# Performance work log

Measured on AMD Instinct MI355X. Metric: run time of the kernel, lower is better.

Reference implementation:

```python
import jax, jax.numpy as jnp
import numpy as np

N_PTS = 1048576
N_FEATS = 32
GRID = (96, 96, 96)
L = 6                      # num_positional_encoding_terms
D_IN = N_FEATS + 2 * L * 3  # 68
H_DIM = 128
VMIN, VMAX = -1.0, 1.0


def setup_inputs() -> dict:
    key = jax.random.key(0)
    ks = jax.random.split(key, 5)
    def lin(k, shp, fan):
        return jax.random.normal(k, shp, jnp.float32) * (1.0 / np.sqrt(fan).astype(np.float32))
    return {
        "x": jax.random.uniform(ks[0], (N_PTS, 3), jnp.float32),          # coords in [0,1) subset of [-1,1]
        "feature_grid": jax.random.uniform(ks[1], (1, N_FEATS) + GRID, jnp.float32),
        "W0": lin(ks[2], (H_DIM, D_IN), D_IN), "b0": jnp.zeros((H_DIM,), jnp.float32),
        "W1": lin(ks[3], (H_DIM, H_DIM), H_DIM), "b1": jnp.zeros((H_DIM,), jnp.float32),
        "W2": lin(ks[4], (1, H_DIM), H_DIM), "b2": jnp.zeros((1,), jnp.float32),
    }


def positional_encoding(x):
    # x: [N, d] -> [N, 2*L*d], NeRF-style: per frequency 2^i * pi, [sin | cos]
    freqs = jnp.pi * (2.0 ** jnp.arange(L, dtype=jnp.float32))   # [L]
    xf = x[:, None, :] * freqs[None, :, None]                    # [N, L, d]
    return jnp.concatenate([jnp.sin(xf), jnp.cos(xf)], axis=-1).reshape(x.shape[0], -1)


def grid_sample_3d(grid, coords):
    # Trilinear F.grid_sample, align_corners=True.
    # grid: [C, D, H, W]; coords: [N, 3] in [-1,1], ordered (x, y, z) -> (W, H, D)
    C, D, H, W = grid.shape
    def unnorm(c, size):
        return (c + 1.0) * 0.5 * (size - 1)
    fx, fy, fz = unnorm(coords[:, 0], W), unnorm(coords[:, 1], H), unnorm(coords[:, 2], D)
    x0, y0, z0 = jnp.floor(fx), jnp.floor(fy), jnp.floor(fz)
    wx, wy, wz = fx - x0, fy - y0, fz - z0
    def ci(i, size):
        return jnp.clip(i.astype(jnp.int32), 0, size - 1)
    x0i, x1i = ci(x0, W), ci(x0 + 1, W)
    y0i, y1i = ci(y0, H), ci(y0 + 1, H)
    z0i, z1i = ci(z0, D), ci(z0 + 1, D)
    def g(zi, yi, xi):
        return grid[:, zi, yi, xi]   # irregular gather -> [C, N]
    return (g(z0i, y0i, x0i) * ((1 - wz) * (1 - wy) * (1 - wx))
          + g(z0i, y0i, x1i) * ((1 - wz) * (1 - wy) * wx)
          + g(z0i, y1i, x0i) * ((1 - wz) * wy * (1 - wx))
          + g(z0i, y1i, x1i) * ((1 - wz) * wy * wx)
          + g(z1i, y0i, x0i) * (wz * (1 - wy) * (1 - wx))
          + g(z1i, y0i, x1i) * (wz * (1 - wy) * wx)
          + g(z1i, y1i, x0i) * (wz * wy * (1 - wx))
          + g(z1i, y1i, x1i) * (wz * wy * wx))   # [C, N]


def reference(x, feature_grid, W0, b0, W1, b1, W2, b2):
    feats = grid_sample_3d(feature_grid[0], x).T                       # [N, C]
    h = jnp.concatenate([positional_encoding(x), feats], axis=1)       # [N, 68]
    h = jax.nn.relu(h @ W0.T + b0)                                     # [N, 128]
    h = jax.nn.relu(h @ W1.T + b1)                                     # [N, 128]
    y = h @ W2.T + b2                                                  # [N, 1]
    return y * (VMAX - VMIN) + VMIN
```

## Files before the change

### kernel.cpp

```cpp
#include <hip/hip_runtime.h>

#define NPTS 1048576
#define NCH 32
#define GS 96
#define GV (GS * GS * GS)
#define DIN 68
#define HD 128
#define TILE_PTS 32
#define NTILES (NPTS / TILE_PTS)
#define NBLK 256
#define NTHR 768
#define WAVES_TOT (NBLK * 12)

typedef __bf16 bf16x8 __attribute__((ext_vector_type(8)));
typedef float f32x4 __attribute__((ext_vector_type(4)));
typedef float f32x2 __attribute__((ext_vector_type(2)));

__device__ __forceinline__ unsigned int f2bf(float f) {
  unsigned int u = __float_as_uint(f);
  return (u + 0x7fffu + ((u >> 16) & 1u)) >> 16;
}
__device__ __forceinline__ unsigned int pkbf(float a, float b) {
  return f2bf(a) | (f2bf(b) << 16);
}

__global__ __launch_bounds__(256) void k_prep_grid(const float* __restrict__ src,
                                                   unsigned int* __restrict__ dst) {
  __shared__ unsigned int tile[256 * 17];
  const int tid = threadIdx.x;
  const long vb = (long)blockIdx.x * 256;
  const int c2 = tid >> 4;
  const int vgb = tid & 15;
#pragma unroll
  for (int p = 0; p < 4; ++p) {
    int vox = (vgb + p * 16) * 4;
    const float4 a = *(const float4*)(src + (long)(2 * c2) * GV + vb + vox);
    const float4 b = *(const float4*)(src + (long)(2 * c2 + 1) * GV + vb + vox);
    tile[(vox + 0) * 17 + c2] = pkbf(a.x, b.x);
    tile[(vox + 1) * 17 + c2] = pkbf(a.y, b.y);
    tile[(vox + 2) * 17 + c2] = pkbf(a.z, b.z);
    tile[(vox + 3) * 17 + c2] = pkbf(a.w, b.w);
  }
  __syncthreads();
  const int vox2 = tid >> 2;
  const int c4 = (tid & 3) * 4;
#pragma unroll
  for (int j = 0; j < 4; ++j) {
    int vx = vox2 + j * 64;
    uint4 w;
    w.x = tile[vx * 17 + c4 + 0];
    w.y = tile[vx * 17 + c4 + 1];
    w.z = tile[vx * 17 + c4 + 2];
    w.w = tile[vx * 17 + c4 + 3];
    *(uint4*)(dst + (vb + vx) * 16 + c4) = w;
  }
}

template <bool TA>
__global__ __launch_bounds__(NTHR, 3) void k_fvsrn(
    const float* __restrict__ X, const float* __restrict__ gridF,
    const unsigned short* __restrict__ gridT,
    const float* __restrict__ W0, const float* __restrict__ B0,
    const float* __restrict__ W1, const float* __restrict__ B1,
    const float* __restrict__ W2, const float* __restrict__ B2,
    float* __restrict__ out) {
  extern __shared__ char smem[];
  float* lb0 = (float*)(smem + 57344);
  float* lb1 = (float*)(smem + 57856);
  float* lw2 = (float*)(smem + 58368);
  const int tid = threadIdx.x;

  for (int idx = tid; idx < 56 * 64; idx += NTHR) {
    int f = idx >> 6;
    int L = idx & 63;
    int qq = L >> 4, lnn = L & 15;
    float vals[8];
    if (f < 24) {
      int kt = f >> 3, nt = f & 7;
      int n = nt * 16 + lnn;
      int kb = kt * 32 + qq * 8;
#pragma unroll
      for (int j = 0; j < 8; ++j) {
        int k = kb + j;
        float w = 0.f;
        if (k < 32) w = W0[n * DIN + 36 + k];
        else if (k < DIN) w = W0[n * DIN + (k - 32)];
        vals[j] = w;
      }
    } else {
      int g = f - 24;
      int kt = g >> 3, nt = g & 7;
      int n = nt * 16 + lnn;
      int kb = kt * 32 + qq * 8;
#pragma unroll
      for (int j = 0; j < 8; ++j) vals[j] = W1[n * HD + kb + j];
    }
    uint4 pk;
    pk.x = pkbf(vals[0], vals[1]);
    pk.y = pkbf(vals[2], vals[3]);
    pk.z = pkbf(vals[4], vals[5]);
    pk.w = pkbf(vals[6], vals[7]);
    *(uint4*)(smem + f * 1024 + L * 16) = pk;
  }
  if (tid < 128) lb0[tid] = B0[tid];
  else if (tid < 256) lb1[tid - 128] = B1[tid - 128];
  else if (tid < 384) lw2[tid - 256] = W2[tid - 256];
  __syncthreads();

  const int wave = tid >> 6, lane = tid & 63;
  char* scr = smem + 58880 + wave * 8192;
  const int q = lane >> 4, ln = lane & 15;
  const int half = lane >> 5, pt = lane & 31;
  const int mtg = pt >> 4, pmg = pt & 15;
  const float b2s = B2[0];

  int t = blockIdx.x * 12 + wave;
  float px = 0.f, py = 0.f, pz = 0.f;
  if (t < NTILES) {
    long p = (long)t * TILE_PTS + pt;
    px = X[p * 3 + 0]; py = X[p * 3 + 1]; pz = X[p * 3 + 2];
  }

  for (; t < NTILES;) {
    const int tn = t + WAVES_TOT;
    const long p0 = (long)t * TILE_PTS;

    float v36[36];
    {
      const float PIf = 3.14159265358979f;
      float cc[3] = {px, py, pz};
#pragma unroll
      for (int ax = 0; ax < 3; ++ax) {
        float s, co;
        __sincosf(PIf * cc[ax], &s, &co);
#pragma unroll
        for (int i = 0; i < 6; ++i) {
          v36[i * 6 + ax] = s;
          v36[i * 6 + 3 + ax] = co;
          float s2 = 2.f * s * co;
          co = 1.f - 2.f * s * s;
          s = s2;
        }
      }
    }
    unsigned int pd[8], e0, e1;
    if (half == 0) {
#pragma unroll
      for (int d = 0; d < 8; ++d) pd[d] = pkbf(v36[2 * d], v36[2 * d + 1]);
      e0 = pkbf(v36[32], v36[33]);
      e1 = pkbf(v36[34], v36[35]);
    } else {
#pragma unroll
      for (int d = 0; d < 8; ++d) pd[d] = pkbf(v36[16 + 2 * d], v36[17 + 2 * d]);
      e0 = 0u; e1 = 0u;
    }

    f32x2 f2[8];
#pragma unroll
    for (int i = 0; i < 8; ++i) f2[i] = (f32x2){0.f, 0.f};
    {
      float fx = (px + 1.f) * 0.5f * (GS - 1);
      float fy = (py + 1.f) * 0.5f * (GS - 1);
      float fz = (pz + 1.f) * 0.5f * (GS - 1);
      float flx = floorf(fx), fly = floorf(fy), flz = floorf(fz);
      float wx = fx - flx, wy = fy - fly, wz = fz - flz;
      int jx = (int)flx, jy = (int)fly, jz = (int)flz;
      int ixa0 = min(max(jx, 0), GS - 1), ixa1 = min(max(jx + 1, 0), GS - 1);
      int iya0 = min(max(jy, 0), GS - 1), iya1 = min(max(jy + 1, 0), GS - 1);
      int iza0 = min(max(jz, 0), GS - 1), iza1 = min(max(jz + 1, 0), GS - 1);
#pragma unroll
      for (int zi = 0; zi < 2; ++zi) {
        int izz = zi ? iza1 : iza0;
        float wzz = zi ? wz : 1.f - wz;
#pragma unroll
        for (int yi = 0; yi < 2; ++yi) {
          int iyy = yi ? iya1 : iya0;
          float wyy = yi ? wy : 1.f - wy;
#pragma unroll
          for (int xi = 0; xi < 2; ++xi) {
            int ixx = xi ? ixa1 : ixa0;
            float w = wzz * wyy * (xi ? wx : 1.f - wx);
            f32x2 w2 = {w, w};
            long vi = ((long)izz * GS + iyy) * GS + ixx;
            if constexpr (TA) {
              const uint4* gp = (const uint4*)(gridT + vi * NCH + 16 * half);
              uint4 g0 = gp[0], g1 = gp[1];
#define ACC_PAIR(u, i)                                                     \
  {                                                                        \
    f32x2 u2 = {__uint_as_float((u) << 16),                                \
                __uint_as_float((u) & 0xffff0000u)};                       \
    f2[i] = __builtin_elementwise_fma(u2, w2, f2[i]);                      \
  }
              ACC_PAIR(g0.x, 0) ACC_PAIR(g0.y, 1) ACC_PAIR(g0.z, 2) ACC_PAIR(g0.w, 3)
              ACC_PAIR(g1.x, 4) ACC_PAIR(g1.y, 5) ACC_PAIR(g1.z, 6) ACC_PAIR(g1.w, 7)
#undef ACC_PAIR
            } else {
#pragma unroll
              for (int i = 0; i < 8; ++i) {
                int c = 16 * half + 2 * i;
                f32x2 u2 = {gridF[(long)c * GV + vi], gridF[(long)(c + 1) * GV + vi]};
                f2[i] = __builtin_elementwise_fma(u2, w2, f2[i]);
              }
            }
          }
        }
      }
    }

    {
      char* fbase = scr + (mtg * 3) * 1024;
      int ro = pmg * 16;
      uint4 s;
      s.x = pkbf(f2[0].x, f2[0].y); s.y = pkbf(f2[1].x, f2[1].y);
      s.z = pkbf(f2[2].x, f2[2].y); s.w = pkbf(f2[3].x, f2[3].y);
      *(uint4*)(fbase + (2 * half) * 256 + ro) = s;
      s.x = pkbf(f2[4].x, f2[4].y); s.y = pkbf(f2[5].x, f2[5].y);
      s.z = pkbf(f2[6].x, f2[6].y); s.w = pkbf(f2[7].x, f2[7].y);
      *(uint4*)(fbase + (2 * half + 1) * 256 + ro) = s;
      s.x = pd[0]; s.y = pd[1]; s.z = pd[2]; s.w = pd[3];
      *(uint4*)(fbase + 1024 + (2 * half) * 256 + ro) = s;
      s.x = pd[4]; s.y = pd[5]; s.z = pd[6]; s.w = pd[7];
      *(uint4*)(fbase + 1024 + (2 * half + 1) * 256 + ro) = s;
      s.x = e0; s.y = e1; s.z = 0u; s.w = 0u;
      *(uint4*)(fbase + 2048 + (2 * half) * 256 + ro) = s;
      s.x = 0u; s.y = 0u; s.z = 0u; s.w = 0u;
      *(uint4*)(fbase + 2048 + (2 * half + 1) * 256 + ro) = s;
    }
    __builtin_amdgcn_wave_barrier();

    if (tn < NTILES) {
      long p = (long)tn * TILE_PTS + pt;
      px = X[p * 3 + 0]; py = X[p * 3 + 1]; pz = X[p * 3 + 2];
    }

    bf16x8 a0[6];
#pragma unroll
    for (int mt = 0; mt < 2; ++mt)
#pragma unroll
      for (int kt = 0; kt < 3; ++kt)
        a0[mt * 3 + kt] = *(const bf16x8*)(scr + (mt * 3 + kt) * 1024 + lane * 16);
    __builtin_amdgcn_wave_barrier();
#pragma unroll
    for (int nt = 0; nt < 8; ++nt) {
      float bn = lb0[nt * 16 + ln];
      f32x4 cinit = {bn, bn, bn, bn};
      f32x4 acc[2];
      acc[0] = cinit; acc[1] = cinit;
#pragma unroll
      for (int kt = 0; kt < 3; ++kt) {
        bf16x8 bfr = *(const bf16x8*)(smem + (kt * 8 + nt) * 1024 + lane * 16);
#pragma unroll
        for (int mt = 0; mt < 2; ++mt)
          acc[mt] = __builtin_amdgcn_mfma_f32_16x16x32_bf16(a0[mt * 3 + kt], bfr, acc[mt], 0, 0, 0);
      }
      int n = nt * 16 + ln;
      int kt1 = n >> 5, j = n & 7, sub = (n >> 3) & 3;
#pragma unroll
      for (int mt = 0; mt < 2; ++mt)
#pragma unroll
        for (int r = 0; r < 4; ++r) {
          float h = fmaxf(acc[mt][r], 0.f);
          *(unsigned short*)(scr + (mt * 4 + kt1) * 1024 + (sub * 16 + q * 4 + r) * 16 + j * 2) =
              (unsigned short)f2bf(h);
        }
    }
    __builtin_amdgcn_wave_barrier();

    bf16x8 a1[8];
#pragma unroll
    for (int mt = 0; mt < 2; ++mt)
#pragma unroll
      for (int kt = 0; kt < 4; ++kt)
        a1[mt * 4 + kt] = *(const bf16x8*)(scr + (mt * 4 + kt) * 1024 + lane * 16);
    __builtin_amdgcn_wave_barrier();
    float y[8];
#pragma unroll
    for (int i = 0; i < 8; ++i) y[i] = 0.f;
#pragma unroll
    for (int nt = 0; nt < 8; ++nt) {
      float bn = lb1[nt * 16 + ln];
      float w2n = lw2[nt * 16 + ln];
      f32x4 cinit = {bn, bn, bn, bn};
      f32x4 acc[2];
      acc[0] = cinit; acc[1] = cinit;
#pragma unroll
      for (int kt = 0; kt < 4; ++kt) {
        bf16x8 bfr = *(const bf16x8*)(smem + 24576 + (kt * 8 + nt) * 1024 + lane * 16);
#pragma unroll
        for (int mt = 0; mt < 2; ++mt)
          acc[mt] = __builtin_amdgcn_mfma_f32_16x16x32_bf16(a1[mt * 4 + kt], bfr, acc[mt], 0, 0, 0);
      }
#pragma unroll
      for (int mt = 0; mt < 2; ++mt)
#pragma unroll
        for (int r = 0; r < 4; ++r)
          y[mt * 4 + r] += w2n * fmaxf(acc[mt][r], 0.f);
    }
#pragma unroll
    for (int i = 0; i < 8; ++i) {
      float v = y[i];
      v += __shfl_xor(v, 1);
      v += __shfl_xor(v, 2);
      v += __shfl_xor(v, 4);
      v += __shfl_xor(v, 8);
      y[i] = v;
    }
    if (ln == 0) {
#pragma unroll
      for (int mt = 0; mt < 2; ++mt)
#pragma unroll
        for (int r = 0; r < 4; ++r)
          out[p0 + mt * 16 + q * 4 + r] = (y[mt * 4 + r] + b2s) * 2.f - 1.f;
    }
    t = tn;
  }
}

extern "C" void kernel_launch(void* const* d_in, const int* in_sizes, int n_in,
                              void* d_out, int out_size, void* d_ws, size_t ws_size,
                              hipStream_t stream) {
  const float* X  = (const float*)d_in[0];
  const float* G  = (const float*)d_in[1];
  const float* W0 = (const float*)d_in[2];
  const float* B0 = (const float*)d_in[3];
  const float* W1 = (const float*)d_in[4];
  const float* B1 = (const float*)d_in[5];
  const float* W2 = (const float*)d_in[6];
  const float* B2 = (const float*)d_in[7];
  float* out = (float*)d_out;

  const size_t needT = (size_t)GV * NCH * 2;
  const size_t shmem = 157184;

  if (ws_size >= needT) {
    k_prep_grid<<<GV / 256, 256, 0, stream>>>(G, (unsigned int*)d_ws);
    k_fvsrn<true><<<NBLK, NTHR, shmem, stream>>>(
        X, G, (const unsigned short*)d_ws, W0, B0, W1, B1, W2, B2, out);
  } else {
    k_fvsrn<false><<<NBLK, NTHR, shmem, stream>>>(
        X, G, (const unsigned short*)nullptr, W0, B0, W1, B1, W2, B2, out);
  }
}
```

Before: 301.1 us.

## Hoist trilinear gathers ahead of encoding, use hardware bf16 pack and sin/cos

```diff
diff --git a/kernel.cpp b/kernel.cpp
--- a/kernel.cpp
+++ b/kernel.cpp
@@ -22,6 +22,11 @@
 }
 __device__ __forceinline__ unsigned int pkbf(float a, float b) {
   return f2bf(a) | (f2bf(b) << 16);
+}
+__device__ __forceinline__ unsigned int cvtpk(float a, float b) {
+  unsigned int r;
+  asm("v_cvt_pk_bf16_f32 %0, %1, %2" : "=v"(r) : "v"(a), "v"(b));
+  return r;
 }
 
 __global__ __launch_bounds__(256) void k_prep_grid(const float* __restrict__ src,
@@ -125,14 +130,56 @@
     const int tn = t + WAVES_TOT;
     const long p0 = (long)t * TILE_PTS;
 
+    uint4 ga[8], gb[8];
+    float w8[8];
+    {
+      float fx = (px + 1.f) * 0.5f * (GS - 1);
+      float fy = (py + 1.f) * 0.5f * (GS - 1);
+      float fz = (pz + 1.f) * 0.5f * (GS - 1);
+      float flx = floorf(fx), fly = floorf(fy), flz = floorf(fz);
+      float wx = fx - flx, wy = fy - fly, wz = fz - flz;
+      int jx = (int)flx, jy = (int)fly, jz = (int)flz;
+      int x0 = min(max(jx, 0), GS - 1), x1 = min(max(jx + 1, 0), GS - 1);
+      int y0 = min(max(jy, 0), GS - 1) * GS, y1 = min(max(jy + 1, 0), GS - 1) * GS;
+      int z0 = min(max(jz, 0), GS - 1) * (GS * GS), z1 = min(max(jz + 1, 0), GS - 1) * (GS * GS);
+      if constexpr (TA) {
+#pragma unroll
+        for (int c = 0; c < 8; ++c) {
+          int vi = (c & 4 ? z1 : z0) + (c & 2 ? y1 : y0) + (c & 1 ? x1 : x0);
+          const uint4* gp = (const uint4*)(gridT + vi * NCH + 16 * half);
+          ga[c] = gp[0];
+          gb[c] = gp[1];
+        }
+      }
+      float ux0 = 1.f - wx, uy0 = 1.f - wy, uz0 = 1.f - wz;
+#pragma unroll
+      for (int c = 0; c < 8; ++c)
+        w8[c] = (c & 4 ? wz : uz0) * (c & 2 ? wy : uy0) * (c & 1 ? wx : ux0);
+      if constexpr (!TA) {
+#pragma unroll
+        for (int c = 0; c < 8; ++c) {
+          int vi = (c & 4 ? z1 : z0) + (c & 2 ? y1 : y0) + (c & 1 ? x1 : x0);
+#pragma unroll
+          for (int i = 0; i < 8; ++i) {
+            int ch = 16 * half + 2 * i;
+            unsigned int lo = f2bf(gridF[(long)ch * GV + vi]);
+            unsigned int hi = f2bf(gridF[(long)(ch + 1) * GV + vi]);
+            if (i < 4) { ((unsigned int*)&ga[c])[i] = lo | (hi << 16); }
+            else       { ((unsigned int*)&gb[c])[i - 4] = lo | (hi << 16); }
+          }
+        }
+      }
+    }
+
     float v36[36];
     {
-      const float PIf = 3.14159265358979f;
       float cc[3] = {px, py, pz};
 #pragma unroll
       for (int ax = 0; ax < 3; ++ax) {
+        float hrev = 0.5f * cc[ax];
         float s, co;
-        __sincosf(PIf * cc[ax], &s, &co);
+        asm("v_sin_f32 %0, %1" : "=v"(s) : "v"(hrev));
+        asm("v_cos_f32 %0, %1" : "=v"(co) : "v"(hrev));
 #pragma unroll
         for (int i = 0; i < 6; ++i) {
           v36[i * 6 + ax] = s;
@@ -146,76 +193,41 @@
     unsigned int pd[8], e0, e1;
     if (half == 0) {
 #pragma unroll
-      for (int d = 0; d < 8; ++d) pd[d] = pkbf(v36[2 * d], v36[2 * d + 1]);
-      e0 = pkbf(v36[32], v36[33]);
-      e1 = pkbf(v36[34], v36[35]);
+      for (int d = 0; d < 8; ++d) pd[d] = cvtpk(v36[2 * d], v36[2 * d + 1]);
+      e0 = cvtpk(v36[32], v36[33]);
+      e1 = cvtpk(v36[34], v36[35]);
     } else {
 #pragma unroll
-      for (int d = 0; d < 8; ++d) pd[d] = pkbf(v36[16 + 2 * d], v36[17 + 2 * d]);
+      for (int d = 0; d < 8; ++d) pd[d] = cvtpk(v36[16 + 2 * d], v36[17 + 2 * d]);
       e0 = 0u; e1 = 0u;
     }
 
     f32x2 f2[8];
 #pragma unroll
     for (int i = 0; i < 8; ++i) f2[i] = (f32x2){0.f, 0.f};
-    {
-      float fx = (px + 1.f) * 0.5f * (GS - 1);
-      float fy = (py + 1.f) * 0.5f * (GS - 1);
-      float fz = (pz + 1.f) * 0.5f * (GS - 1);
-      float flx = floorf(fx), fly = floorf(fy), flz = floorf(fz);
-      float wx = fx - flx, wy = fy - fly, wz = fz - flz;
-      int jx = (int)flx, jy = (int)fly, jz = (int)flz;
-      int ixa0 = min(max(jx, 0), GS - 1), ixa1 = min(max(jx + 1, 0), GS - 1);
-      int iya0 = min(max(jy, 0), GS - 1), iya1 = min(max(jy + 1, 0), GS - 1);
-      int iza0 = min(max(jz, 0), GS - 1), iza1 = min(max(jz + 1, 0), GS - 1);
-#pragma unroll
-      for (int zi = 0; zi < 2; ++zi) {
-        int izz = zi ? iza1 : iza0;
-        float wzz = zi ? wz : 1.f - wz;
-#pragma unroll
-        for (int yi = 0; yi < 2; ++yi) {
-          int iyy = yi ? iya1 : iya0;
-          float wyy = yi ? wy : 1.f - wy;
-#pragma unroll
-          for (int xi = 0; xi < 2; ++xi) {
-            int ixx = xi ? ixa1 : ixa0;
-            float w = wzz * wyy * (xi ? wx : 1.f - wx);
-            f32x2 w2 = {w, w};
-            long vi = ((long)izz * GS + iyy) * GS + ixx;
-            if constexpr (TA) {
-              const uint4* gp = (const uint4*)(gridT + vi * NCH + 16 * half);
-              uint4 g0 = gp[0], g1 = gp[1];
+#pragma unroll
+    for (int c = 0; c < 8; ++c) {
+      f32x2 w2 = {w8[c], w8[c]};
 #define ACC_PAIR(u, i)                                                     \
   {                                                                        \
     f32x2 u2 = {__uint_as_float((u) << 16),                                \
                 __uint_as_float((u) & 0xffff0000u)};                       \
     f2[i] = __builtin_elementwise_fma(u2, w2, f2[i]);                      \
   }
-              ACC_PAIR(g0.x, 0) ACC_PAIR(g0.y, 1) ACC_PAIR(g0.z, 2) ACC_PAIR(g0.w, 3)
-              ACC_PAIR(g1.x, 4) ACC_PAIR(g1.y, 5) ACC_PAIR(g1.z, 6) ACC_PAIR(g1.w, 7)
+      ACC_PAIR(ga[c].x, 0) ACC_PAIR(ga[c].y, 1) ACC_PAIR(ga[c].z, 2) ACC_PAIR(ga[c].w, 3)
+      ACC_PAIR(gb[c].x, 4) ACC_PAIR(gb[c].y, 5) ACC_PAIR(gb[c].z, 6) ACC_PAIR(gb[c].w, 7)
 #undef ACC_PAIR
-            } else {
-#pragma unroll
-              for (int i = 0; i < 8; ++i) {
-                int c = 16 * half + 2 * i;
-                f32x2 u2 = {gridF[(long)c * GV + vi], gridF[(long)(c + 1) * GV + vi]};
-                f2[i] = __builtin_elementwise_fma(u2, w2, f2[i]);
-              }
-            }
-          }
-        }
-      }
     }
 
     {
       char* fbase = scr + (mtg * 3) * 1024;
       int ro = pmg * 16;
       uint4 s;
-      s.x = pkbf(f2[0].x, f2[0].y); s.y = pkbf(f2[1].x, f2[1].y);
-      s.z = pkbf(f2[2].x, f2[2].y); s.w = pkbf(f2[3].x, f2[3].y);
+      s.x = cvtpk(f2[0].x, f2[0].y); s.y = cvtpk(f2[1].x, f2[1].y);
+      s.z = cvtpk(f2[2].x, f2[2].y); s.w = cvtpk(f2[3].x, f2[3].y);
       *(uint4*)(fbase + (2 * half) * 256 + ro) = s;
-      s.x = pkbf(f2[4].x, f2[4].y); s.y = pkbf(f2[5].x, f2[5].y);
-      s.z = pkbf(f2[6].x, f2[6].y); s.w = pkbf(f2[7].x, f2[7].y);
+      s.x = cvtpk(f2[4].x, f2[4].y); s.y = cvtpk(f2[5].x, f2[5].y);
+      s.z = cvtpk(f2[6].x, f2[6].y); s.w = cvtpk(f2[7].x, f2[7].y);
       *(uint4*)(fbase + (2 * half + 1) * 256 + ro) = s;
       s.x = pd[0]; s.y = pd[1]; s.z = pd[2]; s.w = pd[3];
       *(uint4*)(fbase + 1024 + (2 * half) * 256 + ro) = s;
@@ -256,13 +268,17 @@
       int n = nt * 16 + ln;
       int kt1 = n >> 5, j = n & 7, sub = (n >> 3) & 3;
 #pragma unroll
-      for (int mt = 0; mt < 2; ++mt)
-#pragma unroll
-        for (int r = 0; r < 4; ++r) {
-          float h = fmaxf(acc[mt][r], 0.f);
-          *(unsigned short*)(scr + (mt * 4 + kt1) * 1024 + (sub * 16 + q * 4 + r) * 16 + j * 2) =
-              (unsigned short)f2bf(h);
-        }
+      for (int mt = 0; mt < 2; ++mt) {
+        f32x4 zz = {0.f, 0.f, 0.f, 0.f};
+        f32x4 h = __builtin_elementwise_max(acc[mt], zz);
+        char* base = scr + (mt * 4 + kt1) * 1024 + (sub * 16 + q * 4) * 16 + j * 2;
+        unsigned int u01 = cvtpk(h[0], h[1]);
+        unsigned int u23 = cvtpk(h[2], h[3]);
+        *(unsigned short*)(base + 0)  = (unsigned short)u01;
+        *(unsigned short*)(base + 16) = (unsigned short)(u01 >> 16);
+        *(unsigned short*)(base + 32) = (unsigned short)u23;
+        *(unsigned short*)(base + 48) = (unsigned short)(u23 >> 16);
+      }
     }
     __builtin_amdgcn_wave_barrier();
 
```

New measurement: 289.0 us. 1.04x faster.
